# Optimization experiments

Measured on AMD Instinct MI355X. Metric: run time of the kernel, lower is better.

The kernel has to match this reference:

```python
import jax, jax.numpy as jnp
import numpy as np

N, E = 100000, 3200000
F_IN, F_HID, F_OUT = 512, 256, 16
K, ALPHA = 10, 0.1


def setup_inputs() -> dict:
    key = jax.random.key(0)
    k0, k1, k2, k3 = jax.random.split(key, 4)
    x = jax.random.normal(k0, (N, F_IN), dtype=jnp.float32)
    w1 = jax.random.normal(k1, (F_HID, F_IN), dtype=jnp.float32) / np.sqrt(F_IN).astype(np.float32)
    b1 = jnp.zeros((F_HID,), dtype=jnp.float32)
    w2 = jax.random.normal(k2, (F_OUT, F_HID), dtype=jnp.float32) / np.sqrt(F_HID).astype(np.float32)
    b2 = jnp.zeros((F_OUT,), dtype=jnp.float32)
    edge_index = jax.random.randint(k3, (2, E), 0, N, dtype=jnp.int64)
    return {"x": x, "w1": w1, "b1": b1, "w2": w2, "b2": b2, "edge_index": edge_index}


def reference(x, w1, b1, w2, b2, edge_index):
    # MLP (dropout is identity at inference)
    h = jax.nn.relu(x @ w1.T + b1)          # [N, F_HID]
    h = h @ w2.T + b2                        # [N, F_OUT]

    # gcn_norm with self-loops: norm_e = d^-1/2[src] * d^-1/2[dst]
    loop = jnp.arange(N, dtype=edge_index.dtype)
    row = jnp.concatenate([edge_index[0], loop])  # sources, [E+N]
    col = jnp.concatenate([edge_index[1], loop])  # targets, [E+N]
    deg = jax.ops.segment_sum(jnp.ones(row.shape, dtype=h.dtype), col, num_segments=N)
    dinv = jnp.where(deg > 0, jax.lax.rsqrt(jnp.maximum(deg, 1.0)), 0.0)
    norm = (dinv[row] * dinv[col])[:, None]  # [E+N, 1]

    # K-step personalized PageRank: z <- (1-a) * A_hat z + a * h
    def step(z, _):
        agg = jax.ops.segment_sum(norm * z[row], col, num_segments=N)
        return (1.0 - ALPHA) * agg + ALPHA * h, None

    z, _ = jax.lax.scan(step, h, None, length=K)
    return z
```

## Files before the change

kernel.cpp:

```cpp
#include <hip/hip_runtime.h>
#include <stdint.h>

#define F_IN 512
#define F_HID 256
#define F_OUT 16
#define K_STEPS 10
#define NN 100000
#define EE 3200000
#define NB 391
#define CHUNK 8192
#define NCHK ((EE + CHUNK - 1) / CHUNK)

typedef float f32x4 __attribute__((ext_vector_type(4)));
typedef float f32x2 __attribute__((ext_vector_type(2)));
typedef short bf16x8 __attribute__((ext_vector_type(8)));
typedef unsigned int u32;
typedef unsigned int u32x4 __attribute__((ext_vector_type(4)));

__device__ __forceinline__ unsigned short f2bf(float f) {
  unsigned u = __builtin_bit_cast(unsigned, f);
  u += 0x7FFFu + ((u >> 16) & 1u);
  return (unsigned short)(u >> 16);
}
__device__ __forceinline__ float bflo(u32 w) { return __builtin_bit_cast(float, w << 16); }
__device__ __forceinline__ float bfhi(u32 w) { return __builtin_bit_cast(float, w & 0xffff0000u); }
__device__ __forceinline__ int pad_cnt(int deg) { return (deg + 3) & ~3; }

__global__ __launch_bounds__(256) void convert_w1_kernel(const float* __restrict__ w1,
                                                         unsigned short* __restrict__ w1b) {
  int i = blockIdx.x * 256 + threadIdx.x;
  if (i < F_HID * F_IN) w1b[i] = f2bf(w1[i]);
}

__global__ __launch_bounds__(256) void bucket_count_kernel(const int* __restrict__ ei,
                                                           int* __restrict__ bucket_cnt) {
  __shared__ int cntL[512];
  const int tid = threadIdx.x;
  cntL[tid] = 0; cntL[tid + 256] = 0;
  __syncthreads();
  const int base = blockIdx.x * CHUNK;
  int n = EE - base; if (n > CHUNK) n = CHUNK;
  for (int k = tid; k < n; k += 256) {
    int c = ei[EE + base + k];
    atomicAdd(&cntL[c >> 8], 1);
  }
  __syncthreads();
  if (cntL[tid]) atomicAdd(&bucket_cnt[tid], cntL[tid]);
  if (tid + 256 < NB && cntL[tid + 256]) atomicAdd(&bucket_cnt[tid + 256], cntL[tid + 256]);
}

__global__ void alloc_kernel(const int* __restrict__ bucket_cnt,
                             int* __restrict__ ebuf_base, int* __restrict__ csr_base,
                             int* __restrict__ totals,
                             u32* __restrict__ ya, u32* __restrict__ yb) {
  int t = threadIdx.x;
  if (t < NB) {
    int c = bucket_cnt[t];
    ebuf_base[t] = atomicAdd(&totals[0], c);
    csr_base[t]  = atomicAdd(&totals[1], c + 768);
  }
  if (t >= 400 && t < 408) ya[(size_t)NN * 8 + (t - 400)] = 0;
  if (t >= 408 && t < 416) yb[(size_t)NN * 8 + (t - 408)] = 0;
}

__global__ __launch_bounds__(256) void scatter_kernel(const int* __restrict__ ei,
                                                      const int* __restrict__ ebuf_base,
                                                      int* __restrict__ ebuf_fill,
                                                      u32* __restrict__ ebuf) {
  __shared__ u32 sA[512], sB[512], cnt0[512], fillI[512], runb[512];
  __shared__ u32 staged[CHUNK], gaddrL[CHUNK];
  const int tid = threadIdx.x;
  const int base = blockIdx.x * CHUNK;
  int n = EE - base; if (n > CHUNK) n = CHUNK;

  sA[tid] = 0; sA[tid + 256] = 0;
  fillI[tid] = 0; fillI[tid + 256] = 0;
  __syncthreads();
  for (int k = tid; k < n; k += 256) {
    int c = ei[EE + base + k];
    atomicAdd(&sA[c >> 8], 1u);
  }
  __syncthreads();
  cnt0[tid] = sA[tid]; cnt0[tid + 256] = sA[tid + 256];
  __syncthreads();
  u32* src = sA; u32* dst = sB;
  for (int off = 1; off < 512; off <<= 1) {
#pragma unroll
    for (int e = 0; e < 2; ++e) {
      int i = tid + e * 256;
      u32 v = src[i];
      if (i >= off) v += src[i - off];
      dst[i] = v;
    }
    __syncthreads();
    u32* tmp = src; src = dst; dst = tmp;
  }
#pragma unroll
  for (int e = 0; e < 2; ++e) {
    int b = tid + e * 256;
    if (b < NB && cnt0[b] > 0)
      runb[b] = (u32)ebuf_base[b] + (u32)atomicAdd(&ebuf_fill[b], (int)cnt0[b]);
  }
  __syncthreads();
  for (int k = tid; k < n; k += 256) {
    int r = ei[base + k];
    int c = ei[EE + base + k];
    int b = c >> 8;
    u32 excl = src[b] - cnt0[b];
    u32 slot = excl + atomicAdd(&fillI[b], 1u);
    staged[slot] = ((u32)r << 8) | (u32)(c & 255);
    gaddrL[slot] = runb[b] + (slot - excl);
  }
  __syncthreads();
  for (int s = tid; s < n; s += 256) ebuf[gaddrL[s]] = staged[s];
}

__global__ __launch_bounds__(256) void bucket_sort_kernel(const u32* __restrict__ ebuf,
                                                          const int* __restrict__ bucket_cnt,
                                                          const int* __restrict__ ebuf_base,
                                                          const int* __restrict__ csr_base,
                                                          int* __restrict__ node_off,
                                                          int* __restrict__ indeg,
                                                          int* __restrict__ csr_src) {
  __shared__ int degL[256], exclL[256], scT[256], fillL[256];
  __shared__ u32 sorted[10240];
  const int t = threadIdx.x;
  const int b = blockIdx.x;
  const int n0 = b << 8;
  const int nInB = (NN - n0) < 256 ? (NN - n0) : 256;
  const int cnt = bucket_cnt[b];
  const int ebase = ebuf_base[b];
  const int cbase = csr_base[b];

  degL[t] = 0;
  for (int j = t; j < 10240; j += 256) sorted[j] = NN;
  __syncthreads();
  for (int j = t; j < cnt; j += 256) atomicAdd(&degL[(int)(ebuf[ebase + j] & 255u)], 1);
  __syncthreads();
  int deg = degL[t];
  int pcnt = (deg + 3) & ~3;
  scT[t] = pcnt;
  __syncthreads();
  for (int off = 1; off < 256; off <<= 1) {
    int v = (t >= off) ? scT[t - off] : 0;
    __syncthreads();
    scT[t] += v;
    __syncthreads();
  }
  int excl = scT[t] - pcnt;
  exclL[t] = excl;
  fillL[t] = 0;
  int total = scT[255];
  if (t < nInB) {
    node_off[n0 + t] = cbase + excl;
    indeg[n0 + t] = deg;
  }
  __syncthreads();
  for (int j = t; j < cnt; j += 256) {
    u32 e = ebuf[ebase + j];
    int nl = (int)(e & 255u);
    int pos = exclL[nl] + atomicAdd(&fillL[nl], 1);
    sorted[pos] = e >> 8;
  }
  __syncthreads();
  for (int j = t; j < total; j += 256) csr_src[cbase + j] = (int)sorted[j];
}

#define BM 64
#define BKC 32
#define NCH (F_IN / BKC)
#define AST 80
#define BST 80
#define ABYT (BM * AST)
#define BBYT (F_HID * BST)
#define PBYT (ABYT + BBYT)
__global__ __launch_bounds__(256) void mlp_kernel(const float* __restrict__ x,
                                                  const unsigned short* __restrict__ w1b,
                                                  const float* __restrict__ b1,
                                                  const float* __restrict__ w2,
                                                  const float* __restrict__ b2,
                                                  const int* __restrict__ indeg,
                                                  float* __restrict__ hterm,
                                                  u32* __restrict__ y0) {
  __shared__ char lds[2 * PBYT];
  const int tid = threadIdx.x;
  const int wv = tid >> 6, l = tid & 63;
  const int lr = l & 15, lk = l >> 4;
  const int m0 = blockIdx.x * BM;

  const int rowA = tid >> 2, qA = tid & 3;
  int grA = m0 + rowA; if (grA >= NN) grA = NN - 1;
  const float* gA = x + (size_t)grA * F_IN + qA * 8;
  const int lofA = rowA * AST + qA * 16;
  const unsigned short* gB[4];
  int lofB[4];
#pragma unroll
  for (int ib = 0; ib < 4; ++ib) {
    int col = (tid >> 2) + 64 * ib, q = tid & 3;
    gB[ib]  = w1b + (size_t)col * F_IN + q * 8;
    lofB[ib] = ABYT + col * BST + q * 16;
  }

  f32x4 acc[4][4];
#pragma unroll
  for (int a = 0; a < 4; ++a)
#pragma unroll
    for (int b = 0; b < 4; ++b) acc[a][b] = (f32x4){0.f, 0.f, 0.f, 0.f};

  f32x4 pa0 = *(const f32x4*)(gA);
  f32x4 pa1 = *(const f32x4*)(gA + 4);
  bf16x8 rb[4];
#pragma unroll
  for (int ib = 0; ib < 4; ++ib) rb[ib] = *(const bf16x8*)(gB[ib]);
  {
    bf16x8 ab;
#pragma unroll
    for (int j = 0; j < 4; ++j) { ab[j] = (short)f2bf(pa0[j]); ab[j + 4] = (short)f2bf(pa1[j]); }
    *(bf16x8*)(lds + lofA) = ab;
#pragma unroll
    for (int ib = 0; ib < 4; ++ib) *(bf16x8*)(lds + lofB[ib]) = rb[ib];
  }
  __syncthreads();

  for (int c = 0; c < NCH; ++c) {
    char* buf = lds + (c & 1) * PBYT;
    if (c < NCH - 1) {
      pa0 = *(const f32x4*)(gA + (c + 1) * BKC);
      pa1 = *(const f32x4*)(gA + (c + 1) * BKC + 4);
#pragma unroll
      for (int ib = 0; ib < 4; ++ib) rb[ib] = *(const bf16x8*)(gB[ib] + (c + 1) * BKC);
    }
    bf16x8 af[4], bfr[4];
#pragma unroll
    for (int fm = 0; fm < 4; ++fm)
      af[fm] = *(const bf16x8*)(buf + (fm * 16 + lr) * AST + lk * 16);
#pragma unroll
    for (int fn = 0; fn < 4; ++fn)
      bfr[fn] = *(const bf16x8*)(buf + ABYT + (wv * 64 + fn * 16 + lr) * BST + lk * 16);
#pragma unroll
    for (int fm = 0; fm < 4; ++fm)
#pragma unroll
      for (int fn = 0; fn < 4; ++fn)
        acc[fm][fn] = __builtin_amdgcn_mfma_f32_16x16x32_bf16(af[fm], bfr[fn], acc[fm][fn],
                                                              0, 0, 0);
    if (c < NCH - 1) {
      char* nbuf = lds + ((c + 1) & 1) * PBYT;
      bf16x8 ab;
#pragma unroll
      for (int j = 0; j < 4; ++j) { ab[j] = (short)f2bf(pa0[j]); ab[j + 4] = (short)f2bf(pa1[j]); }
      *(bf16x8*)(nbuf + lofA) = ab;
#pragma unroll
      for (int ib = 0; ib < 4; ++ib) *(bf16x8*)(nbuf + lofB[ib]) = rb[ib];
    }
    __syncthreads();
  }

  unsigned short* h1p = (unsigned short*)lds;
  unsigned short* w2p = (unsigned short*)(lds + 64 * 264 * 2);
#pragma unroll
  for (int fn = 0; fn < 4; ++fn) {
    int col = wv * 64 + fn * 16 + lr;
    float bb = b1[col];
#pragma unroll
    for (int fm = 0; fm < 4; ++fm) {
#pragma unroll
      for (int r = 0; r < 4; ++r) {
        float v = acc[fm][fn][r] + bb;
        v = v > 0.f ? v : 0.f;
        h1p[(fm * 16 + lk * 4 + r) * 264 + col] = f2bf(v);
      }
    }
  }
  for (int i = tid; i < 16 * 256; i += 256) w2p[(i >> 8) * 264 + (i & 255)] = f2bf(w2[i]);
  __syncthreads();

  f32x4 acc2 = (f32x4){0.f, 0.f, 0.f, 0.f};
#pragma unroll
  for (int ks = 0; ks < 8; ++ks) {
    bf16x8 a2 = *(const bf16x8*)&h1p[(wv * 16 + lr) * 264 + ks * 32 + lk * 8];
    bf16x8 b2f = *(const bf16x8*)&w2p[lr * 264 + ks * 32 + lk * 8];
    acc2 = __builtin_amdgcn_mfma_f32_16x16x32_bf16(a2, b2f, acc2, 0, 0, 0);
  }
  float bb2 = b2[lr];
#pragma unroll
  for (int r = 0; r < 4; ++r) {
    int row = m0 + wv * 16 + lk * 4 + r;
    if (row < NN) {
      float d = (float)(indeg[row] + 1);
      float di = rsqrtf(d);
      float v = (acc2[r] + bb2) * di;
      hterm[(size_t)row * F_OUT + lr] = 0.1f * v;
      float vo = __shfl_xor(v, 1, 64);
      if ((lr & 1) == 0) {
        u32 pw = (u32)f2bf(v) | ((u32)f2bf(vo) << 16);
        y0[(size_t)row * 8 + (lr >> 1)] = pw;
      }
    }
  }
}

__global__ __launch_bounds__(256) void ppr_kernel(const int* __restrict__ node_off,
                                                  const int* __restrict__ indeg,
                                                  const int* __restrict__ csr_src,
                                                  const u32* __restrict__ yin,
                                                  const float* __restrict__ hterm,
                                                  u32* __restrict__ yout) {
  int t = blockIdx.x * 256 + threadIdx.x;
  int g = t >> 3, f2 = t & 7;
  if (g >= NN) return;
  const int lane = threadIdx.x & 63;
  const int gb = lane & 56;
  const int es = f2 >> 1, hf = f2 & 1;

  int deg = indeg[g], s0 = node_off[g];
  int pc = pad_cnt(deg);

  float al[4] = {0.f, 0.f, 0.f, 0.f};
  float ah[4] = {0.f, 0.f, 0.f, 0.f};

  int sa = (pc > 0) ? csr_src[s0 + (f2 & 3)] : 0;
  for (int base = 0; base < pc; base += 4) {
    int nxt = (base + 4 < pc) ? base + 4 : base;
    int sa_n = csr_src[s0 + nxt + (f2 & 3)];
    int na = __shfl(sa, gb + es, 64);
    u32x4 v = *(const u32x4*)(yin + (size_t)na * 8 + hf * 4);
#pragma unroll
    for (int j = 0; j < 4; ++j) {
      al[j] += bflo(v[j]);
      ah[j] += bfhi(v[j]);
    }
    sa = sa_n;
  }
#pragma unroll
  for (int j = 0; j < 4; ++j) {
    al[j] += __shfl_xor(al[j], 2, 64);
    ah[j] += __shfl_xor(ah[j], 2, 64);
    al[j] += __shfl_xor(al[j], 4, 64);
    ah[j] += __shfl_xor(ah[j], 4, 64);
  }
  if (es == 0) {
    u32x4 sv = *(const u32x4*)(yin + (size_t)g * 8 + hf * 4);
    float ra = 0.9f * __builtin_amdgcn_rcpf((float)(deg + 1));
    f32x4 ht0 = *(const f32x4*)(hterm + (size_t)g * F_OUT + hf * 8);
    f32x4 ht1 = *(const f32x4*)(hterm + (size_t)g * F_OUT + hf * 8 + 4);
    u32x4 o;
#pragma unroll
    for (int j = 0; j < 4; ++j) {
      float lo = ra * (al[j] + bflo(sv[j]));
      float hi = ra * (ah[j] + bfhi(sv[j]));
      lo += (j < 2) ? ht0[2 * j] : ht1[2 * j - 4];
      hi += (j < 2) ? ht0[2 * j + 1] : ht1[2 * j - 3];
      o[j] = (u32)f2bf(lo) | ((u32)f2bf(hi) << 16);
    }
    *(u32x4*)(yout + (size_t)g * 8 + hf * 4) = o;
  }
}

__global__ __launch_bounds__(256) void out_kernel(const u32* __restrict__ y,
                                                  const int* __restrict__ indeg,
                                                  float* __restrict__ out) {
  int t = blockIdx.x * 256 + threadIdx.x;
  if (t >= NN * 8) return;
  float sd = sqrtf((float)(indeg[t >> 3] + 1));
  u32 w = y[t];
  f32x2 o = {bflo(w) * sd, bfhi(w) * sd};
  *(f32x2*)(out + (size_t)t * 2) = o;
}

extern "C" void kernel_launch(void* const* d_in, const int* in_sizes, int n_in,
                              void* d_out, int out_size, void* d_ws, size_t ws_size,
                              hipStream_t stream) {
  const float* x  = (const float*)d_in[0];
  const float* w1 = (const float*)d_in[1];
  const float* b1 = (const float*)d_in[2];
  const float* w2 = (const float*)d_in[3];
  const float* b2 = (const float*)d_in[4];
  const int*   ei = (const int*)d_in[5];

  char* p = (char*)d_ws;
  auto alloc = [&](size_t bytes) {
    char* r = p;
    p += (bytes + 255) & ~(size_t)255;
    return r;
  };
  float* hterm = (float*)alloc((size_t)NN * F_OUT * 4);
  u32* ya = (u32*)alloc((size_t)(NN + 1) * 8 * 4);
  u32* yb = (u32*)alloc((size_t)(NN + 1) * 8 * 4);
  unsigned short* w1b = (unsigned short*)alloc((size_t)F_HID * F_IN * 2);
  int* aux = (int*)alloc(((size_t)2 * NB + 2) * 4);
  int* bucket_cnt = aux;
  int* ebuf_fill  = aux + NB;
  int* totals     = aux + 2 * NB;
  int* ebuf_base = (int*)alloc((size_t)NB * 4);
  int* csr_base  = (int*)alloc((size_t)NB * 4);
  int* node_off  = (int*)alloc((size_t)NN * 4);
  int* indeg     = (int*)alloc((size_t)NN * 4);
  u32* ebuf      = (u32*)alloc((size_t)EE * 4);
  int* csr_src   = (int*)alloc(((size_t)EE + (size_t)NB * 768) * 4);

  hipMemsetAsync(aux, 0, ((size_t)2 * NB + 2) * 4, stream);

  convert_w1_kernel<<<(F_HID * F_IN + 255) / 256, 256, 0, stream>>>(w1, w1b);
  bucket_count_kernel<<<NCHK, 256, 0, stream>>>(ei, bucket_cnt);
  alloc_kernel<<<1, 512, 0, stream>>>(bucket_cnt, ebuf_base, csr_base, totals, ya, yb);
  scatter_kernel<<<NCHK, 256, 0, stream>>>(ei, ebuf_base, ebuf_fill, ebuf);
  bucket_sort_kernel<<<NB, 256, 0, stream>>>(ebuf, bucket_cnt, ebuf_base, csr_base,
                                             node_off, indeg, csr_src);
  mlp_kernel<<<(NN + BM - 1) / BM, 256, 0, stream>>>(x, w1b, b1, w2, b2, indeg, hterm, ya);

  u32* yin = ya;
  u32* yout = yb;
  for (int k = 0; k < K_STEPS; ++k) {
    ppr_kernel<<<((size_t)NN * 8 + 255) / 256, 256, 0, stream>>>(node_off, indeg, csr_src,
                                                                 yin, hterm, yout);
    u32* tmp = yin; yin = yout; yout = tmp;
  }
  out_kernel<<<((size_t)NN * 8 + 255) / 256, 256, 0, stream>>>(yin, indeg, (float*)d_out);
}
```

Baseline: 458.4 us.

## Degree-sorted node permutation, 4 lanes per node, and bf16 hterm in PPR

The bucket sort now also builds a per-bucket permutation that orders nodes by padded degree, so PPR wavefronts process nodes of similar degree and lose less time to load imbalance. The PPR kernel switches from 8 to 4 lanes per node and pads CSR rows to 8, so each lane loads its 4 source indices as one vector and issues 4 gathers per block. The alpha*h term is stored in bf16 to halve its traffic. In exchange there is an extra indirection through perm, more CSR padding, and some added bf16 rounding in the h term.

Result: faster. 443.4 us (-3.3%).

```diff
diff --git a/kernel.cpp b/kernel.cpp
--- a/kernel.cpp
+++ b/kernel.cpp
@@ -24,7 +24,6 @@
 }
 __device__ __forceinline__ float bflo(u32 w) { return __builtin_bit_cast(float, w << 16); }
 __device__ __forceinline__ float bfhi(u32 w) { return __builtin_bit_cast(float, w & 0xffff0000u); }
-__device__ __forceinline__ int pad_cnt(int deg) { return (deg + 3) & ~3; }
 
 __global__ __launch_bounds__(256) void convert_w1_kernel(const float* __restrict__ w1,
                                                          unsigned short* __restrict__ w1b) {
@@ -57,7 +56,7 @@
   if (t < NB) {
     int c = bucket_cnt[t];
     ebuf_base[t] = atomicAdd(&totals[0], c);
-    csr_base[t]  = atomicAdd(&totals[1], c + 768);
+    csr_base[t]  = atomicAdd(&totals[1], ((c + 7) & ~7) + 2048);
   }
   if (t >= 400 && t < 408) ya[(size_t)NN * 8 + (t - 400)] = 0;
   if (t >= 408 && t < 416) yb[(size_t)NN * 8 + (t - 408)] = 0;
@@ -121,9 +120,11 @@
                                                           const int* __restrict__ csr_base,
                                                           int* __restrict__ node_off,
                                                           int* __restrict__ indeg,
-                                                          int* __restrict__ csr_src) {
+                                                          int* __restrict__ csr_src,
+                                                          int* __restrict__ perm) {
   __shared__ int degL[256], exclL[256], scT[256], fillL[256];
-  __shared__ u32 sorted[10240];
+  __shared__ int binc[64], bino[64], binf[64];
+  __shared__ u32 sorted[12288];
   const int t = threadIdx.x;
   const int b = blockIdx.x;
   const int n0 = b << 8;
@@ -133,12 +134,13 @@
   const int cbase = csr_base[b];
 
   degL[t] = 0;
-  for (int j = t; j < 10240; j += 256) sorted[j] = NN;
+  if (t < 64) { binc[t] = 0; binf[t] = 0; }
+  for (int j = t; j < 12288; j += 256) sorted[j] = NN;
   __syncthreads();
   for (int j = t; j < cnt; j += 256) atomicAdd(&degL[(int)(ebuf[ebase + j] & 255u)], 1);
   __syncthreads();
   int deg = degL[t];
-  int pcnt = (deg + 3) & ~3;
+  int pcnt = (deg + 7) & ~7;
   scT[t] = pcnt;
   __syncthreads();
   for (int off = 1; off < 256; off <<= 1) {
@@ -155,7 +157,15 @@
     node_off[n0 + t] = cbase + excl;
     indeg[n0 + t] = deg;
   }
-  __syncthreads();
+  int key = pcnt >> 3; if (key > 63) key = 63;
+  if (t < nInB) atomicAdd(&binc[key], 1);
+  __syncthreads();
+  if (t == 0) { int s = 0; for (int k2 = 0; k2 < 64; ++k2) { bino[k2] = s; s += binc[k2]; } }
+  __syncthreads();
+  if (t < nInB) {
+    int rank = bino[key] + atomicAdd(&binf[key], 1);
+    perm[n0 + rank] = n0 + t;
+  }
   for (int j = t; j < cnt; j += 256) {
     u32 e = ebuf[ebase + j];
     int nl = (int)(e & 255u);
@@ -180,7 +190,7 @@
                                                   const float* __restrict__ w2,
                                                   const float* __restrict__ b2,
                                                   const int* __restrict__ indeg,
-                                                  float* __restrict__ hterm,
+                                                  u32* __restrict__ htermp,
                                                   u32* __restrict__ y0) {
   __shared__ char lds[2 * PBYT];
   const int tid = threadIdx.x;
@@ -289,11 +299,11 @@
       float d = (float)(indeg[row] + 1);
       float di = rsqrtf(d);
       float v = (acc2[r] + bb2) * di;
-      hterm[(size_t)row * F_OUT + lr] = 0.1f * v;
       float vo = __shfl_xor(v, 1, 64);
       if ((lr & 1) == 0) {
-        u32 pw = (u32)f2bf(v) | ((u32)f2bf(vo) << 16);
-        y0[(size_t)row * 8 + (lr >> 1)] = pw;
+        y0[(size_t)row * 8 + (lr >> 1)] = (u32)f2bf(v) | ((u32)f2bf(vo) << 16);
+        htermp[(size_t)row * 8 + (lr >> 1)] =
+            (u32)f2bf(0.1f * v) | ((u32)f2bf(0.1f * vo) << 16);
       }
     }
   }
@@ -301,55 +311,52 @@
 
 __global__ __launch_bounds__(256) void ppr_kernel(const int* __restrict__ node_off,
                                                   const int* __restrict__ indeg,
+                                                  const int* __restrict__ perm,
                                                   const int* __restrict__ csr_src,
                                                   const u32* __restrict__ yin,
-                                                  const float* __restrict__ hterm,
+                                                  const u32* __restrict__ htermp,
                                                   u32* __restrict__ yout) {
   int t = blockIdx.x * 256 + threadIdx.x;
-  int g = t >> 3, f2 = t & 7;
-  if (g >= NN) return;
-  const int lane = threadIdx.x & 63;
-  const int gb = lane & 56;
-  const int es = f2 >> 1, hf = f2 & 1;
-
-  int deg = indeg[g], s0 = node_off[g];
-  int pc = pad_cnt(deg);
+  int i = t >> 2;
+  if (i >= NN) return;
+  const int sub = t & 3, eo = sub >> 1, hf = sub & 1;
+  const int g = perm[i];
+  const int deg = indeg[g], s0 = node_off[g];
+  const int nblk = ((deg + 7) & ~7) >> 3;
 
   float al[4] = {0.f, 0.f, 0.f, 0.f};
   float ah[4] = {0.f, 0.f, 0.f, 0.f};
 
-  int sa = (pc > 0) ? csr_src[s0 + (f2 & 3)] : 0;
-  for (int base = 0; base < pc; base += 4) {
-    int nxt = (base + 4 < pc) ? base + 4 : base;
-    int sa_n = csr_src[s0 + nxt + (f2 & 3)];
-    int na = __shfl(sa, gb + es, 64);
-    u32x4 v = *(const u32x4*)(yin + (size_t)na * 8 + hf * 4);
+  const u32* cp = (const u32*)csr_src + s0 + eo * 4;
+  u32x4 sidx;
+  if (nblk > 0) sidx = *(const u32x4*)cp;
+  for (int b = 0; b < nblk; ++b) {
+    u32x4 snxt;
+    if (b + 1 < nblk) snxt = *(const u32x4*)(cp + (size_t)(b + 1) * 8);
 #pragma unroll
     for (int j = 0; j < 4; ++j) {
-      al[j] += bflo(v[j]);
-      ah[j] += bfhi(v[j]);
-    }
-    sa = sa_n;
+      u32x4 v = *(const u32x4*)(yin + (size_t)sidx[j] * 8 + hf * 4);
+      al[0] += bflo(v[0]); ah[0] += bfhi(v[0]);
+      al[1] += bflo(v[1]); ah[1] += bfhi(v[1]);
+      al[2] += bflo(v[2]); ah[2] += bfhi(v[2]);
+      al[3] += bflo(v[3]); ah[3] += bfhi(v[3]);
+    }
+    sidx = snxt;
   }
 #pragma unroll
   for (int j = 0; j < 4; ++j) {
     al[j] += __shfl_xor(al[j], 2, 64);
     ah[j] += __shfl_xor(ah[j], 2, 64);
-    al[j] += __shfl_xor(al[j], 4, 64);
-    ah[j] += __shfl_xor(ah[j], 4, 64);
-  }
-  if (es == 0) {
+  }
+  if (eo == 0) {
     u32x4 sv = *(const u32x4*)(yin + (size_t)g * 8 + hf * 4);
+    u32x4 hp = *(const u32x4*)(htermp + (size_t)g * 8 + hf * 4);
     float ra = 0.9f * __builtin_amdgcn_rcpf((float)(deg + 1));
-    f32x4 ht0 = *(const f32x4*)(hterm + (size_t)g * F_OUT + hf * 8);
-    f32x4 ht1 = *(const f32x4*)(hterm + (size_t)g * F_OUT + hf * 8 + 4);
     u32x4 o;
 #pragma unroll
     for (int j = 0; j < 4; ++j) {
-      float lo = ra * (al[j] + bflo(sv[j]));
-      float hi = ra * (ah[j] + bfhi(sv[j]));
-      lo += (j < 2) ? ht0[2 * j] : ht1[2 * j - 4];
-      hi += (j < 2) ? ht0[2 * j + 1] : ht1[2 * j - 3];
+      float lo = ra * (al[j] + bflo(sv[j])) + bflo(hp[j]);
+      float hi = ra * (ah[j] + bfhi(sv[j])) + bfhi(hp[j]);
       o[j] = (u32)f2bf(lo) | ((u32)f2bf(hi) << 16);
     }
     *(u32x4*)(yout + (size_t)g * 8 + hf * 4) = o;
@@ -383,7 +390,7 @@
     p += (bytes + 255) & ~(size_t)255;
     return r;
   };
-  float* hterm = (float*)alloc((size_t)NN * F_OUT * 4);
+  u32* htermp = (u32*)alloc((size_t)NN * 8 * 4);
   u32* ya = (u32*)alloc((size_t)(NN + 1) * 8 * 4);
   u32* yb = (u32*)alloc((size_t)(NN + 1) * 8 * 4);
   unsigned short* w1b = (unsigned short*)alloc((size_t)F_HID * F_IN * 2);
@@ -395,8 +402,9 @@
   int* csr_base  = (int*)alloc((size_t)NB * 4);
   int* node_off  = (int*)alloc((size_t)NN * 4);
   int* indeg     = (int*)alloc((size_t)NN * 4);
+  int* perm      = (int*)alloc((size_t)NN * 4);
   u32* ebuf      = (u32*)alloc((size_t)EE * 4);
-  int* csr_src   = (int*)alloc(((size_t)EE + (size_t)NB * 768) * 4);
+  int* csr_src   = (int*)alloc(((size_t)EE + (size_t)NB * 2048 + 64) * 4);
 
   hipMemsetAsync(aux, 0, ((size_t)2 * NB + 2) * 4, stream);
 
@@ -405,14 +413,14 @@
   alloc_kernel<<<1, 512, 0, stream>>>(bucket_cnt, ebuf_base, csr_base, totals, ya, yb);
   scatter_kernel<<<NCHK, 256, 0, stream>>>(ei, ebuf_base, ebuf_fill, ebuf);
   bucket_sort_kernel<<<NB, 256, 0, stream>>>(ebuf, bucket_cnt, ebuf_base, csr_base,
-                                             node_off, indeg, csr_src);
-  mlp_kernel<<<(NN + BM - 1) / BM, 256, 0, stream>>>(x, w1b, b1, w2, b2, indeg, hterm, ya);
+                                             node_off, indeg, csr_src, perm);
+  mlp_kernel<<<(NN + BM - 1) / BM, 256, 0, stream>>>(x, w1b, b1, w2, b2, indeg, htermp, ya);
 
   u32* yin = ya;
   u32* yout = yb;
   for (int k = 0; k < K_STEPS; ++k) {
-    ppr_kernel<<<((size_t)NN * 8 + 255) / 256, 256, 0, stream>>>(node_off, indeg, csr_src,
-                                                                 yin, hterm, yout);
+    ppr_kernel<<<((size_t)NN * 4 + 255) / 256, 256, 0, stream>>>(node_off, indeg, perm,
+                                                                 csr_src, yin, htermp, yout);
     u32* tmp = yin; yin = yout; yout = tmp;
   }
   out_kernel<<<((size_t)NN * 8 + 255) / 256, 256, 0, stream>>>(yin, indeg, (float*)d_out);
```
